# Optimization experiments

Hardware: AMD Instinct MI355X
Metric: run time of the kernel (lower is better)

## Reference

```python
import jax, jax.numpy as jnp
import numpy as np

BS, SLEN, DIM, HID, E, TOPK = 4, 2048, 2048, 1792, 8, 2


def setup_inputs() -> dict:
    key = jax.random.key(0)
    ks = jax.random.split(key, 9)
    s = 0.02  # trunc_normal-style init scale
    return {
        "x": jax.random.normal(ks[0], (BS, SLEN, DIM), jnp.float32),
        "gate_w": jax.random.normal(ks[1], (DIM, E), jnp.float32) * s,
        "w1": jax.random.normal(ks[2], (E, DIM, HID), jnp.float32) * s,
        "w2": jax.random.normal(ks[3], (E, HID, DIM), jnp.float32) * s,
        "w3": jax.random.normal(ks[4], (E, DIM, HID), jnp.float32) * s,
        "sw1": jax.random.normal(ks[5], (DIM, HID), jnp.float32) * s,
        "sw2": jax.random.normal(ks[6], (HID, DIM), jnp.float32) * s,
        "sw3": jax.random.normal(ks[7], (DIM, HID), jnp.float32) * s,
        "expert_bias": jnp.zeros((E,), jnp.float32),
    }


def reference(x, gate_w, w1, w2, w3, sw1, sw2, sw3, expert_bias):
    bs, slen, dim = x.shape
    T = bs * slen
    xf = x.reshape(T, dim)

    # --- TokenChoiceTopKRouter ---
    scores = jax.nn.softmax((xf @ gate_w).astype(jnp.float32), axis=-1)  # [T, E]
    _, sel = jax.lax.top_k(scores + expert_bias[None, :], TOPK)          # [T, K] expert ids
    top_scores = jnp.take_along_axis(scores, sel, axis=1)                # [T, K] (bias-free scores)
    flat_sel = sel.reshape(-1)                                           # [T*K]
    counts = jnp.bincount(flat_sel, length=E).astype(jnp.int32)          # tokens per expert
    order = jnp.argsort(flat_sel, stable=True)                           # group tokens by expert
    top_scores_sorted = top_scores.reshape(-1)[order]                    # [T*K]
    token_idx = order // TOPK                                            # source token per routed row

    # --- dispatch: gather + scale by router weight ---
    routed_in = xf[token_idx] * top_scores_sorted[:, None]               # [T*K, dim]

    # --- GroupedExperts: grouped GEMM SiLU-gated FFN ---
    h = jax.nn.silu(jax.lax.ragged_dot(routed_in, w1, counts)) \
        * jax.lax.ragged_dot(routed_in, w3, counts)                      # [T*K, hid]
    routed_out = jax.lax.ragged_dot(h, w2, counts)                       # [T*K, dim]

    # --- shared expert (single-expert FFN over all tokens) ---
    out = (jax.nn.silu(xf @ sw1) * (xf @ sw3)) @ sw2                     # [T, dim]

    # --- combine: scatter-add routed outputs back to tokens ---
    out = out.at[token_idx].add(routed_out)
    return out.reshape(bs, slen, dim)
```

## Files before the change

kernel.cpp:

```cpp
#include <hip/hip_runtime.h>

typedef unsigned short u16;
typedef unsigned int u32;

#define TOK   8192
#define DIMK  2048
#define HIDN  1792
#define NEXP  8
#define NPAIR 16384
#define MAXROWS 17408
#define MAXTILES 136

typedef float f32x4 __attribute__((ext_vector_type(4)));
typedef __bf16 bf16x8 __attribute__((ext_vector_type(8)));

__device__ __forceinline__ u16 f2bf(float f) {
    u32 u = __float_as_uint(f);
    u += 0x7fffu + ((u >> 16) & 1u);
    return (u16)(u >> 16);
}

__device__ __forceinline__ void gll16(const void* g, void* l) {
    __builtin_amdgcn_global_load_lds((__attribute__((address_space(1))) void*)(g),
                                     (__attribute__((address_space(3))) void*)(l),
                                     16, 0, 0);
}

__global__ void transpose_f2bf(const float* __restrict__ In, u16* __restrict__ Out,
                               int R, int C) {
    __shared__ float tile[64 * 65];
    size_t moff = (size_t)blockIdx.z * R * C;
    const float* in = In + moff;
    u16* out = Out + moff;
    int c0 = blockIdx.x * 64, r0 = blockIdx.y * 64;
    int tid = threadIdx.x;
#pragma unroll
    for (int p = 0; p < 16; ++p) {
        int idx = tid + p * 256;
        int r = idx >> 6, c = idx & 63;
        tile[r * 65 + c] = in[(size_t)(r0 + r) * C + c0 + c];
    }
    __syncthreads();
#pragma unroll
    for (int p = 0; p < 8; ++p) {
        int idx = (tid + p * 256) * 2;
        int ro = idx >> 6;
        int co = idx & 63;
        float v0 = tile[co * 65 + ro];
        float v1 = tile[(co + 1) * 65 + ro];
        u32 u = (u32)f2bf(v0) | ((u32)f2bf(v1) << 16);
        *(u32*)&out[(size_t)(c0 + ro) * R + r0 + co] = u;
    }
}

__global__ void cvt_f2bf(const float* __restrict__ in, u16* __restrict__ out, int n8) {
    int i = blockIdx.x * 256 + threadIdx.x;
    if (i >= n8) return;
    const float4* p = (const float4*)in;
    float4 a = p[2 * i], b = p[2 * i + 1];
    union { u16 us[8]; uint4 u4; } o;
    o.us[0] = f2bf(a.x); o.us[1] = f2bf(a.y); o.us[2] = f2bf(a.z); o.us[3] = f2bf(a.w);
    o.us[4] = f2bf(b.x); o.us[5] = f2bf(b.y); o.us[6] = f2bf(b.z); o.us[7] = f2bf(b.w);
    ((uint4*)out)[i] = o.u4;
}

__global__ void router_k(const float* __restrict__ x, const float* __restrict__ gw,
                         const float* __restrict__ ebias, int* __restrict__ sel,
                         float* __restrict__ scor, int* __restrict__ pos,
                         int* __restrict__ counts) {
    int wave = threadIdx.x >> 6, lane = threadIdx.x & 63;
    int t = blockIdx.x * 4 + wave;
    const float* xr = x + (size_t)t * DIMK;
    float acc[8];
#pragma unroll
    for (int e = 0; e < 8; ++e) acc[e] = 0.f;
    for (int i = lane; i < DIMK; i += 64) {
        float xv = xr[i];
        float4 g0 = *(const float4*)(gw + (size_t)i * 8);
        float4 g1 = *(const float4*)(gw + (size_t)i * 8 + 4);
        acc[0] += xv * g0.x; acc[1] += xv * g0.y; acc[2] += xv * g0.z; acc[3] += xv * g0.w;
        acc[4] += xv * g1.x; acc[5] += xv * g1.y; acc[6] += xv * g1.z; acc[7] += xv * g1.w;
    }
#pragma unroll
    for (int off = 32; off; off >>= 1)
#pragma unroll
        for (int e = 0; e < 8; ++e) acc[e] += __shfl_xor(acc[e], off, 64);
    if (lane == 0) {
        float mx = acc[0];
#pragma unroll
        for (int e = 1; e < 8; ++e) mx = fmaxf(mx, acc[e]);
        float pv[8], psum = 0.f;
#pragma unroll
        for (int e = 0; e < 8; ++e) { pv[e] = __expf(acc[e] - mx); psum += pv[e]; }
        float inv = 1.f / psum;
        float bb[8];
#pragma unroll
        for (int e = 0; e < 8; ++e) { pv[e] *= inv; bb[e] = pv[e] + ebias[e]; }
        int e0 = 0;
#pragma unroll
        for (int e = 1; e < 8; ++e) if (bb[e] > bb[e0]) e0 = e;
        int e1 = (e0 == 0) ? 1 : 0;
#pragma unroll
        for (int e = 0; e < 8; ++e) if (e != e0 && bb[e] > bb[e1]) e1 = e;
        int i0 = t * 2, i1 = t * 2 + 1;
        sel[i0] = e0; sel[i1] = e1;
        scor[i0] = pv[e0]; scor[i1] = pv[e1];
        pos[i0] = atomicAdd(&counts[e0], 1);
        pos[i1] = atomicAdd(&counts[e1], 1);
    }
}

__global__ void scan_k(const int* __restrict__ counts, int* __restrict__ seg,
                       int* __restrict__ tile_e, int* __restrict__ tile_r0,
                       int* __restrict__ ntile) {
    if (threadIdx.x == 0 && blockIdx.x == 0) {
        int off = 0, nt = 0;
        for (int e = 0; e < NEXP; ++e) {
            seg[e] = off;
            int c = counts[e];
            int tiles = (c + 127) >> 7;
            for (int j = 0; j < tiles; ++j) { tile_e[nt] = e; tile_r0[nt] = off + (j << 7); ++nt; }
            off += tiles << 7;
        }
        *ntile = nt;
    }
}

__global__ void dispatch_k(const float* __restrict__ x, const int* __restrict__ sel,
                           const float* __restrict__ scor, const int* __restrict__ pos,
                           const int* __restrict__ counts, const int* __restrict__ seg,
                           u32* __restrict__ rin, int* __restrict__ tok) {
    int b = blockIdx.x;
    if (b < NPAIR) {
        int t = b >> 1;
        int e = sel[b];
        float s = scor[b];
        int row = seg[e] + pos[b];
        const float2* xr = (const float2*)(x + (size_t)t * DIMK);
        u32* orow = rin + (size_t)row * (DIMK / 2);
        for (int i = threadIdx.x; i < DIMK / 2; i += 256) {
            float2 v = xr[i];
            orow[i] = (u32)f2bf(v.x * s) | ((u32)f2bf(v.y * s) << 16);
        }
        if (threadIdx.x == 0) tok[row] = t;
    } else {
        int pb = b - NPAIR;
        int e = pb >> 7, j = pb & 127;
        int c = counts[e];
        int al = (c + 127) & ~127;
        if (c + j < al) {
            int row = seg[e] + c + j;
            u32* orow = rin + (size_t)row * (DIMK / 2);
            for (int i = threadIdx.x; i < DIMK / 2; i += 256) orow[i] = 0u;
            if (threadIdx.x == 0) tok[row] = -1;
        }
    }
}

template <bool GROUPED>
__launch_bounds__(256, 2)
__global__ void gemm_h(const u16* __restrict__ A, const u16* __restrict__ B1g,
                       const u16* __restrict__ B3g, u16* __restrict__ H,
                       const int* __restrict__ tile_e, const int* __restrict__ tile_r0,
                       const int* __restrict__ ntile) {
    constexpr int Kd = DIMK;
    constexpr int Nd = HIDN;
    __shared__ u16 As[128 * 32];
    __shared__ u16 B1s[128 * 32];
    __shared__ u16 B3s[128 * 32];
    int bx = blockIdx.x;
    int r0; size_t woff = 0;
    if constexpr (GROUPED) {
        if (bx >= *ntile) return;
        r0 = tile_r0[bx];
        woff = (size_t)tile_e[bx] * (size_t)Nd * Kd;
    } else {
        r0 = bx * 128;
    }
    int c0 = blockIdx.y * 128;
    int tid = threadIdx.x, wave = tid >> 6, lane = tid & 63;
    int srow = wave * 16 + (lane >> 2);
    int skc = (lane & 3) * 8;
    const u16* gA0 = A + (size_t)(r0 + srow) * Kd + skc;
    const u16* gA1 = gA0 + (size_t)64 * Kd;
    const u16* gB1a = B1g + woff + (size_t)(c0 + srow) * Kd + skc;
    const u16* gB1b = gB1a + (size_t)64 * Kd;
    const u16* gB3a = B3g + woff + (size_t)(c0 + srow) * Kd + skc;
    const u16* gB3b = gB3a + (size_t)64 * Kd;
    char* lA0 = (char*)As + wave * 1024;   char* lA1 = (char*)As + 4096 + wave * 1024;
    char* lB1a = (char*)B1s + wave * 1024; char* lB1b = (char*)B1s + 4096 + wave * 1024;
    char* lB3a = (char*)B3s + wave * 1024; char* lB3b = (char*)B3s + 4096 + wave * 1024;

    int wr = wave >> 1, wc = wave & 1;
    int fr = lane & 15, fq = lane >> 4;
    const u16* fA = As + (wr * 64 + fr) * 32 + fq * 8;
    const u16* fB1 = B1s + (wc * 64 + fr) * 32 + fq * 8;
    const u16* fB3 = B3s + (wc * 64 + fr) * 32 + fq * 8;

    f32x4 acc1[4][4], acc3[4][4];
    f32x4 zz = {0.f, 0.f, 0.f, 0.f};
#pragma unroll
    for (int m = 0; m < 4; ++m)
#pragma unroll
        for (int n = 0; n < 4; ++n) { acc1[m][n] = zz; acc3[m][n] = zz; }

    for (int kt = 0; kt < Kd / 32; ++kt) {
        int ko = kt * 32;
        gll16(gA0 + ko, lA0);  gll16(gA1 + ko, lA1);
        gll16(gB1a + ko, lB1a); gll16(gB1b + ko, lB1b);
        gll16(gB3a + ko, lB3a); gll16(gB3b + ko, lB3b);
        __syncthreads();
        bf16x8 aF[4], b1F[4], b3F[4];
#pragma unroll
        for (int m = 0; m < 4; ++m) aF[m] = *(const bf16x8*)(fA + m * 16 * 32);
#pragma unroll
        for (int n = 0; n < 4; ++n) {
            b1F[n] = *(const bf16x8*)(fB1 + n * 16 * 32);
            b3F[n] = *(const bf16x8*)(fB3 + n * 16 * 32);
        }
#pragma unroll
        for (int m = 0; m < 4; ++m)
#pragma unroll
            for (int n = 0; n < 4; ++n) {
                acc1[m][n] = __builtin_amdgcn_mfma_f32_16x16x32_bf16(aF[m], b1F[n], acc1[m][n], 0, 0, 0);
                acc3[m][n] = __builtin_amdgcn_mfma_f32_16x16x32_bf16(aF[m], b3F[n], acc3[m][n], 0, 0, 0);
            }
        __syncthreads();
    }
#pragma unroll
    for (int m = 0; m < 4; ++m) {
#pragma unroll
        for (int n = 0; n < 4; ++n) {
            int gcol = c0 + wc * 64 + n * 16 + fr;
#pragma unroll
            for (int i = 0; i < 4; ++i) {
                int grow = r0 + wr * 64 + m * 16 + fq * 4 + i;
                float p1 = acc1[m][n][i], p3 = acc3[m][n][i];
                float h = p1 * p3 / (1.f + __expf(-p1));
                H[(size_t)grow * Nd + gcol] = f2bf(h);
            }
        }
    }
}

template <int MODE>
__launch_bounds__(256, 2)
__global__ void gemm_o(const u16* __restrict__ A, const u16* __restrict__ Bg,
                       float* __restrict__ Out,
                       const int* __restrict__ tile_e, const int* __restrict__ tile_r0,
                       const int* __restrict__ ntile, const int* __restrict__ tok) {
    constexpr int Kd = HIDN;
    constexpr int Nd = DIMK;
    __shared__ u16 As[128 * 32];
    __shared__ u16 Bs[128 * 32];
    int bx = blockIdx.x;
    int r0; size_t woff = 0;
    if constexpr (MODE == 1) {
        if (bx >= *ntile) return;
        r0 = tile_r0[bx];
        woff = (size_t)tile_e[bx] * (size_t)Nd * Kd;
    } else {
        r0 = bx * 128;
    }
    int c0 = blockIdx.y * 128;
    int tid = threadIdx.x, wave = tid >> 6, lane = tid & 63;
    int srow = wave * 16 + (lane >> 2);
    int skc = (lane & 3) * 8;
    const u16* gA0 = A + (size_t)(r0 + srow) * Kd + skc;
    const u16* gA1 = gA0 + (size_t)64 * Kd;
    const u16* gB0 = Bg + woff + (size_t)(c0 + srow) * Kd + skc;
    const u16* gB1 = gB0 + (size_t)64 * Kd;
    char* lA0 = (char*)As + wave * 1024; char* lA1 = (char*)As + 4096 + wave * 1024;
    char* lB0 = (char*)Bs + wave * 1024; char* lB1 = (char*)Bs + 4096 + wave * 1024;
    int wr = wave >> 1, wc = wave & 1;
    int fr = lane & 15, fq = lane >> 4;
    const u16* fA = As + (wr * 64 + fr) * 32 + fq * 8;
    const u16* fB = Bs + (wc * 64 + fr) * 32 + fq * 8;
    f32x4 acc[4][4];
    f32x4 zz = {0.f, 0.f, 0.f, 0.f};
#pragma unroll
    for (int m = 0; m < 4; ++m)
#pragma unroll
        for (int n = 0; n < 4; ++n) acc[m][n] = zz;
    for (int kt = 0; kt < Kd / 32; ++kt) {
        int ko = kt * 32;
        gll16(gA0 + ko, lA0); gll16(gA1 + ko, lA1);
        gll16(gB0 + ko, lB0); gll16(gB1 + ko, lB1);
        __syncthreads();
        bf16x8 aF[4], bF[4];
#pragma unroll
        for (int m = 0; m < 4; ++m) aF[m] = *(const bf16x8*)(fA + m * 16 * 32);
#pragma unroll
        for (int n = 0; n < 4; ++n) bF[n] = *(const bf16x8*)(fB + n * 16 * 32);
#pragma unroll
        for (int m = 0; m < 4; ++m)
#pragma unroll
            for (int n = 0; n < 4; ++n)
                acc[m][n] = __builtin_amdgcn_mfma_f32_16x16x32_bf16(aF[m], bF[n], acc[m][n], 0, 0, 0);
        __syncthreads();
    }
#pragma unroll
    for (int m = 0; m < 4; ++m) {
        int tkv[4];
        if constexpr (MODE == 1) {
#pragma unroll
            for (int i = 0; i < 4; ++i) tkv[i] = tok[r0 + wr * 64 + m * 16 + fq * 4 + i];
        }
#pragma unroll
        for (int n = 0; n < 4; ++n) {
            int gcol = c0 + wc * 64 + n * 16 + fr;
#pragma unroll
            for (int i = 0; i < 4; ++i) {
                float v = acc[m][n][i];
                if constexpr (MODE == 0) {
                    int grow = r0 + wr * 64 + m * 16 + fq * 4 + i;
                    Out[(size_t)grow * Nd + gcol] = v;
                } else {
                    int t2 = tkv[i];
                    if (t2 >= 0) atomicAdd(&Out[(size_t)t2 * Nd + gcol], v);
                }
            }
        }
    }
}

extern "C" void kernel_launch(void* const* d_in, const int* in_sizes, int n_in,
                              void* d_out, int out_size, void* d_ws, size_t ws_size,
                              hipStream_t stream) {
    const float* x    = (const float*)d_in[0];
    const float* gw   = (const float*)d_in[1];
    const float* w1   = (const float*)d_in[2];
    const float* w2   = (const float*)d_in[3];
    const float* w3   = (const float*)d_in[4];
    const float* sw1  = (const float*)d_in[5];
    const float* sw2  = (const float*)d_in[6];
    const float* sw3  = (const float*)d_in[7];
    const float* ebias= (const float*)d_in[8];
    float* out = (float*)d_out;

    char* p = (char*)d_ws;
    auto alloc = [&](size_t b) -> char* {
        char* r = p; p += (b + 255) & ~(size_t)255; return r;
    };
    u16* w1b  = (u16*)alloc((size_t)NEXP * HIDN * DIMK * 2);
    u16* w3b  = (u16*)alloc((size_t)NEXP * HIDN * DIMK * 2);
    u16* w2b  = (u16*)alloc((size_t)NEXP * DIMK * HIDN * 2);
    u16* sw1b = (u16*)alloc((size_t)HIDN * DIMK * 2);
    u16* sw3b = (u16*)alloc((size_t)HIDN * DIMK * 2);
    u16* sw2b = (u16*)alloc((size_t)DIMK * HIDN * 2);
    u16* xb   = (u16*)alloc((size_t)TOK * DIMK * 2);
    u16* rin  = (u16*)alloc((size_t)MAXROWS * DIMK * 2);
    u16* hbuf = (u16*)alloc((size_t)MAXROWS * HIDN * 2);
    int* sel    = (int*)alloc(NPAIR * 4);
    float* scor = (float*)alloc(NPAIR * 4);
    int* pos    = (int*)alloc(NPAIR * 4);
    int* counts = (int*)alloc(64);
    int* seg    = (int*)alloc(64);
    int* tile_e = (int*)alloc(256 * 4);
    int* tile_r0= (int*)alloc(256 * 4);
    int* ntile  = (int*)alloc(64);
    int* tok    = (int*)alloc(MAXROWS * 4);

    hipMemsetAsync(counts, 0, NEXP * 4, stream);

    transpose_f2bf<<<dim3(HIDN / 64, DIMK / 64, NEXP), 256, 0, stream>>>(w1, w1b, DIMK, HIDN);
    transpose_f2bf<<<dim3(HIDN / 64, DIMK / 64, NEXP), 256, 0, stream>>>(w3, w3b, DIMK, HIDN);
    transpose_f2bf<<<dim3(DIMK / 64, HIDN / 64, NEXP), 256, 0, stream>>>(w2, w2b, HIDN, DIMK);
    transpose_f2bf<<<dim3(HIDN / 64, DIMK / 64, 1), 256, 0, stream>>>(sw1, sw1b, DIMK, HIDN);
    transpose_f2bf<<<dim3(HIDN / 64, DIMK / 64, 1), 256, 0, stream>>>(sw3, sw3b, DIMK, HIDN);
    transpose_f2bf<<<dim3(DIMK / 64, HIDN / 64, 1), 256, 0, stream>>>(sw2, sw2b, HIDN, DIMK);

    cvt_f2bf<<<(TOK * DIMK / 8 + 255) / 256, 256, 0, stream>>>(x, xb, TOK * DIMK / 8);
    router_k<<<TOK / 4, 256, 0, stream>>>(x, gw, ebias, sel, scor, pos, counts);
    scan_k<<<1, 64, 0, stream>>>(counts, seg, tile_e, tile_r0, ntile);
    dispatch_k<<<NPAIR + NEXP * 128, 256, 0, stream>>>(x, sel, scor, pos, counts, seg,
                                                       (u32*)rin, tok);

    gemm_h<false><<<dim3(TOK / 128, HIDN / 128), 256, 0, stream>>>(
        xb, sw1b, sw3b, hbuf, nullptr, nullptr, nullptr);
    gemm_o<0><<<dim3(TOK / 128, DIMK / 128), 256, 0, stream>>>(
        hbuf, sw2b, out, nullptr, nullptr, nullptr, nullptr);

    gemm_h<true><<<dim3(MAXTILES, HIDN / 128), 256, 0, stream>>>(
        rin, w1b, w3b, hbuf, tile_e, tile_r0, ntile);
    gemm_o<1><<<dim3(MAXTILES, DIMK / 128), 256, 0, stream>>>(
        hbuf, w2b, out, tile_e, tile_r0, ntile, tok);
}
```

Baseline: 1.440 ms.

## Replace GEMMs with 256x256 pipelined kernel, interleaved w1/w3 and merged shared expert

Replaces the four 128x128 GEMM kernels with one templated 256x256-tile, 512-thread GEMM. It double-buffers LDS with direct global-to-LDS loads and XOR swizzling, and splits each k-step into phases separated by barriers and setprio. w1 and w3 are interleaved in 16-row groups into one concatenated weight, so a single B stream yields both gate and up products. The shared expert is treated as a ninth expert, so it shares the grouped launch for the first layer. The intent is better data reuse and MFMA utilization. The cost is larger padding (256-row tiles), more LDS per block and heavier register pressure.

```diff
diff --git a/kernel.cpp b/kernel.cpp
--- a/kernel.cpp
+++ b/kernel.cpp
@@ -3,13 +3,15 @@
 typedef unsigned short u16;
 typedef unsigned int u32;
 
-#define TOK   8192
-#define DIMK  2048
-#define HIDN  1792
-#define NEXP  8
-#define NPAIR 16384
-#define MAXROWS 17408
-#define MAXTILES 136
+#define TOK    8192
+#define DIMK   2048
+#define HIDN   1792
+#define NCAT   3584
+#define NEXP   8
+#define NPAIR  16384
+#define RROWS  18432
+#define CROWS  26624
+#define MAXMT  104
 
 typedef float f32x4 __attribute__((ext_vector_type(4)));
 typedef __bf16 bf16x8 __attribute__((ext_vector_type(8)));
@@ -19,7 +21,6 @@
     u += 0x7fffu + ((u >> 16) & 1u);
     return (u16)(u >> 16);
 }
-
 __device__ __forceinline__ void gll16(const void* g, void* l) {
     __builtin_amdgcn_global_load_lds((__attribute__((address_space(1))) void*)(g),
                                      (__attribute__((address_space(3))) void*)(l),
@@ -27,11 +28,11 @@
 }
 
 __global__ void transpose_f2bf(const float* __restrict__ In, u16* __restrict__ Out,
-                               int R, int C) {
+                               int R, int C, size_t in_z, size_t out_z, size_t out_off,
+                               int ilv) {
     __shared__ float tile[64 * 65];
-    size_t moff = (size_t)blockIdx.z * R * C;
-    const float* in = In + moff;
-    u16* out = Out + moff;
+    const float* in = In + (size_t)blockIdx.z * in_z;
+    u16* out = Out + (size_t)blockIdx.z * out_z + out_off;
     int c0 = blockIdx.x * 64, r0 = blockIdx.y * 64;
     int tid = threadIdx.x;
 #pragma unroll
@@ -49,7 +50,9 @@
         float v0 = tile[co * 65 + ro];
         float v1 = tile[(co + 1) * 65 + ro];
         u32 u = (u32)f2bf(v0) | ((u32)f2bf(v1) << 16);
-        *(u32*)&out[(size_t)(c0 + ro) * R + r0 + co] = u;
+        int orow = c0 + ro;
+        if (ilv) orow = ((orow & ~15) << 1) + (ilv == 2 ? 16 : 0) + (orow & 15);
+        *(u32*)&out[(size_t)orow * R + r0 + co] = u;
     }
 }
 
@@ -111,18 +114,21 @@
 }
 
 __global__ void scan_k(const int* __restrict__ counts, int* __restrict__ seg,
-                       int* __restrict__ tile_e, int* __restrict__ tile_r0,
-                       int* __restrict__ ntile) {
+                       int* __restrict__ mt_e, int* __restrict__ mt_r0,
+                       int* __restrict__ nmt, int* __restrict__ nrows) {
     if (threadIdx.x == 0 && blockIdx.x == 0) {
-        int off = 0, nt = 0;
+        int ntl = 0;
+        for (int i = 0; i < TOK / 256; ++i) { mt_e[ntl] = 8; mt_r0[ntl] = i * 256; ++ntl; }
+        int off = TOK;
         for (int e = 0; e < NEXP; ++e) {
             seg[e] = off;
             int c = counts[e];
-            int tiles = (c + 127) >> 7;
-            for (int j = 0; j < tiles; ++j) { tile_e[nt] = e; tile_r0[nt] = off + (j << 7); ++nt; }
-            off += tiles << 7;
-        }
-        *ntile = nt;
+            int tl = (c + 255) >> 8;
+            for (int j = 0; j < tl; ++j) { mt_e[ntl] = e; mt_r0[ntl] = off + (j << 8); ++ntl; }
+            off += tl << 8;
+        }
+        *nmt = ntl;
+        *nrows = off;
     }
 }
 
@@ -137,7 +143,7 @@
         float s = scor[b];
         int row = seg[e] + pos[b];
         const float2* xr = (const float2*)(x + (size_t)t * DIMK);
-        u32* orow = rin + (size_t)row * (DIMK / 2);
+        u32* orow = rin + (size_t)(row - TOK) * (DIMK / 2);
         for (int i = threadIdx.x; i < DIMK / 2; i += 256) {
             float2 v = xr[i];
             orow[i] = (u32)f2bf(v.x * s) | ((u32)f2bf(v.y * s) << 16);
@@ -145,180 +151,175 @@
         if (threadIdx.x == 0) tok[row] = t;
     } else {
         int pb = b - NPAIR;
-        int e = pb >> 7, j = pb & 127;
+        int e = pb >> 8, j = pb & 255;
         int c = counts[e];
-        int al = (c + 127) & ~127;
+        int al = (c + 255) & ~255;
         if (c + j < al) {
             int row = seg[e] + c + j;
-            u32* orow = rin + (size_t)row * (DIMK / 2);
+            u32* orow = rin + (size_t)(row - TOK) * (DIMK / 2);
             for (int i = threadIdx.x; i < DIMK / 2; i += 256) orow[i] = 0u;
             if (threadIdx.x == 0) tok[row] = -1;
         }
     }
 }
 
-template <bool GROUPED>
-__launch_bounds__(256, 2)
-__global__ void gemm_h(const u16* __restrict__ A, const u16* __restrict__ B1g,
-                       const u16* __restrict__ B3g, u16* __restrict__ H,
-                       const int* __restrict__ tile_e, const int* __restrict__ tile_r0,
-                       const int* __restrict__ ntile) {
-    constexpr int Kd = DIMK;
-    constexpr int Nd = HIDN;
-    __shared__ u16 As[128 * 32];
-    __shared__ u16 B1s[128 * 32];
-    __shared__ u16 B3s[128 * 32];
-    int bx = blockIdx.x;
-    int r0; size_t woff = 0;
-    if constexpr (GROUPED) {
-        if (bx >= *ntile) return;
-        r0 = tile_r0[bx];
-        woff = (size_t)tile_e[bx] * (size_t)Nd * Kd;
+#define LDA(mh, b) { \
+    _Pragma("unroll") for (int m_ = 0; m_ < 4; ++m_) \
+    _Pragma("unroll") for (int ks_ = 0; ks_ < 2; ++ks_) \
+        aF[mh][m_][ks_] = *(const bf16x8*)(&lds[b][0][0] + aRd + ((mh)*4 + m_) * 2048 + ks_ * 64); }
+#define LDB(nh, b) { \
+    _Pragma("unroll") for (int n_ = 0; n_ < 2; ++n_) \
+    _Pragma("unroll") for (int ks_ = 0; ks_ < 2; ++ks_) \
+        bF[n_][ks_] = *(const bf16x8*)(&lds[b][1][0] + bRd + ((nh)*2 + n_) * 2048 + ks_ * 64); }
+#define MFMAQ(mh, nh) { \
+    _Pragma("unroll") for (int m_ = 0; m_ < 4; ++m_) \
+    _Pragma("unroll") for (int n_ = 0; n_ < 2; ++n_) \
+    _Pragma("unroll") for (int ks_ = 0; ks_ < 2; ++ks_) \
+        acc[(mh)*4 + m_][(nh)*2 + n_] = __builtin_amdgcn_mfma_f32_16x16x32_bf16( \
+            aF[mh][m_][ks_], bF[n_][ks_], acc[(mh)*4 + m_][(nh)*2 + n_], 0, 0, 0); }
+#define SA(kt, half, b) do { \
+    const char* s_ = gA + (size_t)(half) * (128 * ABS) + (size_t)(kt) * 128; \
+    char* d_ = &lds[b][0][0] + (half) * 16384 + t16; \
+    gll16(s_, d_); gll16(s_ + 64 * ABS, d_ + 8192); } while (0)
+#define SB(kt, half, b) do { \
+    const char* s_ = gB + (size_t)(half) * (128 * BBS) + (size_t)(kt) * 128; \
+    char* d_ = &lds[b][1][0] + (half) * 16384 + t16; \
+    gll16(s_, d_); gll16(s_ + 64 * BBS, d_ + 8192); } while (0)
+#define PH_SYNC() \
+    __builtin_amdgcn_s_barrier(); \
+    asm volatile("s_waitcnt lgkmcnt(0)" ::: "memory"); \
+    __builtin_amdgcn_sched_barrier(0); \
+    __builtin_amdgcn_s_setprio(1)
+#define PH_END() \
+    __builtin_amdgcn_s_setprio(0); \
+    __builtin_amdgcn_s_barrier()
+
+template <int KD, int ND, int ASTR, int EPI>
+__launch_bounds__(512, 2)
+__global__ void gemm256(const u16* __restrict__ A0, const u16* __restrict__ A1,
+                        const u16* __restrict__ Bcat, void* __restrict__ Obase,
+                        const int* __restrict__ mt_e, const int* __restrict__ mt_r0,
+                        const int* __restrict__ nmt, const int* __restrict__ tok,
+                        int tile_off) {
+    int my = blockIdx.y + tile_off;
+    if (my >= *nmt) return;
+    const int e = mt_e[my];
+    const int r0 = mt_r0[my];
+    const int c0 = blockIdx.x * 256;
+
+    const u16* Ab;
+    if constexpr (EPI == 0)
+        Ab = (r0 < TOK) ? (A0 + (size_t)r0 * ASTR) : (A1 + (size_t)(r0 - TOK) * ASTR);
+    else
+        Ab = A0 + (size_t)r0 * ASTR;
+    const u16* Bb = Bcat + (size_t)e * ND * KD + (size_t)c0 * KD;
+
+    __shared__ char lds[2][2][32768];
+
+    const int t = threadIdx.x;
+    const int lane = t & 63;
+    const int wid = t >> 6;
+    const int wr = wid >> 2, wc = wid & 3;
+    const int fr = lane & 15, fq = lane >> 4;
+    const int sbit = ((fr >> 2) & 1) << 5;
+    const int aRd = ((wr * 128 + fr) * 128 + fq * 16) ^ sbit;
+    const int bRd = ((wc * 64 + fr) * 128 + fq * 16) ^ sbit;
+    const int t16 = t * 16;
+    constexpr size_t ABS = (size_t)ASTR * 2;
+    constexpr size_t BBS = (size_t)KD * 2;
+    const int scb = ((t & 7) * 16) ^ (((t >> 5) & 1) << 5);
+    const char* gA = (const char*)Ab + (size_t)(t >> 3) * ABS + scb;
+    const char* gB = (const char*)Bb + (size_t)(t >> 3) * BBS + scb;
+
+    f32x4 acc[8][4];
+    const f32x4 zz = {0.f, 0.f, 0.f, 0.f};
+#pragma unroll
+    for (int m = 0; m < 8; ++m)
+#pragma unroll
+        for (int n = 0; n < 4; ++n) acc[m][n] = zz;
+    bf16x8 aF[2][4][2], bF[2][2];
+
+    constexpr int NT = KD / 64;
+    constexpr int NITER = NT / 2;
+
+    SA(0, 0, 0); SA(0, 1, 0); SB(0, 0, 0); SB(0, 1, 0);
+    SA(1, 0, 1); SA(1, 1, 1);
+    asm volatile("s_waitcnt vmcnt(4)" ::: "memory");
+    __builtin_amdgcn_s_barrier();
+
+#pragma unroll 1
+    for (int it = 0; it < NITER; ++it) {
+        const int t0 = 2 * it;
+        const bool pf = (t0 + 2 < NT);
+        LDA(0, 0); LDB(0, 0);
+        SB(t0 + 1, 0, 1);
+        PH_SYNC(); MFMAQ(0, 0); PH_END();
+        LDA(1, 0);
+        SB(t0 + 1, 1, 1);
+        PH_SYNC(); MFMAQ(1, 0); PH_END();
+        LDB(1, 0);
+        if (pf) SA(t0 + 2, 0, 0);
+        PH_SYNC(); MFMAQ(0, 1); PH_END();
+        if (pf) { SA(t0 + 2, 1, 0); asm volatile("s_waitcnt vmcnt(4)" ::: "memory"); }
+        else    { asm volatile("s_waitcnt vmcnt(0)" ::: "memory"); }
+        PH_SYNC(); MFMAQ(1, 1); PH_END();
+        LDA(0, 1); LDB(0, 1);
+        if (pf) SB(t0 + 2, 0, 0);
+        PH_SYNC(); MFMAQ(0, 0); PH_END();
+        LDA(1, 1);
+        if (pf) SB(t0 + 2, 1, 0);
+        PH_SYNC(); MFMAQ(1, 0); PH_END();
+        LDB(1, 1);
+        if (pf) SA(t0 + 3, 0, 1);
+        PH_SYNC(); MFMAQ(0, 1); PH_END();
+        if (pf) { SA(t0 + 3, 1, 1); asm volatile("s_waitcnt vmcnt(4)" ::: "memory"); }
+        PH_SYNC(); MFMAQ(1, 1); PH_END();
+    }
+
+    if constexpr (EPI == 0) {
+        u16* H = (u16*)Obase;
+        constexpr int HST = ND / 2;
+#pragma unroll
+        for (int m = 0; m < 8; ++m) {
+#pragma unroll
+            for (int n = 0; n < 4; n += 2) {
+                int gc = (c0 + wc * 64 + n * 16) / 2 + fr;
+#pragma unroll
+                for (int i = 0; i < 4; ++i) {
+                    int gr = r0 + wr * 128 + m * 16 + fq * 4 + i;
+                    float p1 = acc[m][n][i], p3 = acc[m][n + 1][i];
+                    float h = p1 * p3 / (1.f + __expf(-p1));
+                    H[(size_t)gr * HST + gc] = f2bf(h);
+                }
+            }
+        }
+    } else if constexpr (EPI == 1) {
+        float* O = (float*)Obase;
+#pragma unroll
+        for (int m = 0; m < 8; ++m)
+#pragma unroll
+            for (int n = 0; n < 4; ++n) {
+                int gc = c0 + wc * 64 + n * 16 + fr;
+#pragma unroll
+                for (int i = 0; i < 4; ++i) {
+                    int gr = r0 + wr * 128 + m * 16 + fq * 4 + i;
+                    O[(size_t)gr * ND + gc] = acc[m][n][i];
+                }
+            }
     } else {
-        r0 = bx * 128;
-    }
-    int c0 = blockIdx.y * 128;
-    int tid = threadIdx.x, wave = tid >> 6, lane = tid & 63;
-    int srow = wave * 16 + (lane >> 2);
-    int skc = (lane & 3) * 8;
-    const u16* gA0 = A + (size_t)(r0 + srow) * Kd + skc;
-    const u16* gA1 = gA0 + (size_t)64 * Kd;
-    const u16* gB1a = B1g + woff + (size_t)(c0 + srow) * Kd + skc;
-    const u16* gB1b = gB1a + (size_t)64 * Kd;
-    const u16* gB3a = B3g + woff + (size_t)(c0 + srow) * Kd + skc;
-    const u16* gB3b = gB3a + (size_t)64 * Kd;
-    char* lA0 = (char*)As + wave * 1024;   char* lA1 = (char*)As + 4096 + wave * 1024;
-    char* lB1a = (char*)B1s + wave * 1024; char* lB1b = (char*)B1s + 4096 + wave * 1024;
-    char* lB3a = (char*)B3s + wave * 1024; char* lB3b = (char*)B3s + 4096 + wave * 1024;
-
-    int wr = wave >> 1, wc = wave & 1;
-    int fr = lane & 15, fq = lane >> 4;
-    const u16* fA = As + (wr * 64 + fr) * 32 + fq * 8;
-    const u16* fB1 = B1s + (wc * 64 + fr) * 32 + fq * 8;
-    const u16* fB3 = B3s + (wc * 64 + fr) * 32 + fq * 8;
-
-    f32x4 acc1[4][4], acc3[4][4];
-    f32x4 zz = {0.f, 0.f, 0.f, 0.f};
-#pragma unroll
-    for (int m = 0; m < 4; ++m)
-#pragma unroll
-        for (int n = 0; n < 4; ++n) { acc1[m][n] = zz; acc3[m][n] = zz; }
-
-    for (int kt = 0; kt < Kd / 32; ++kt) {
-        int ko = kt * 32;
-        gll16(gA0 + ko, lA0);  gll16(gA1 + ko, lA1);
-        gll16(gB1a + ko, lB1a); gll16(gB1b + ko, lB1b);
-        gll16(gB3a + ko, lB3a); gll16(gB3b + ko, lB3b);
-        __syncthreads();
-        bf16x8 aF[4], b1F[4], b3F[4];
-#pragma unroll
-        for (int m = 0; m < 4; ++m) aF[m] = *(const bf16x8*)(fA + m * 16 * 32);
-#pragma unroll
-        for (int n = 0; n < 4; ++n) {
-            b1F[n] = *(const bf16x8*)(fB1 + n * 16 * 32);
-            b3F[n] = *(const bf16x8*)(fB3 + n * 16 * 32);
-        }
-#pragma unroll
-        for (int m = 0; m < 4; ++m)
+        float* O = (float*)Obase;
+#pragma unroll
+        for (int m = 0; m < 8; ++m) {
+            int tk[4];
+#pragma unroll
+            for (int i = 0; i < 4; ++i)
+                tk[i] = tok[r0 + wr * 128 + m * 16 + fq * 4 + i];
 #pragma unroll
             for (int n = 0; n < 4; ++n) {
-                acc1[m][n] = __builtin_amdgcn_mfma_f32_16x16x32_bf16(aF[m], b1F[n], acc1[m][n], 0, 0, 0);
-                acc3[m][n] = __builtin_amdgcn_mfma_f32_16x16x32_bf16(aF[m], b3F[n], acc3[m][n], 0, 0, 0);
-            }
-        __syncthreads();
-    }
-#pragma unroll
-    for (int m = 0; m < 4; ++m) {
-#pragma unroll
-        for (int n = 0; n < 4; ++n) {
-            int gcol = c0 + wc * 64 + n * 16 + fr;
-#pragma unroll
-            for (int i = 0; i < 4; ++i) {
-                int grow = r0 + wr * 64 + m * 16 + fq * 4 + i;
-                float p1 = acc1[m][n][i], p3 = acc3[m][n][i];
-                float h = p1 * p3 / (1.f + __expf(-p1));
-                H[(size_t)grow * Nd + gcol] = f2bf(h);
-            }
-        }
-    }
-}
-
-template <int MODE>
-__launch_bounds__(256, 2)
-__global__ void gemm_o(const u16* __restrict__ A, const u16* __restrict__ Bg,
-                       float* __restrict__ Out,
-                       const int* __restrict__ tile_e, const int* __restrict__ tile_r0,
-                       const int* __restrict__ ntile, const int* __restrict__ tok) {
-    constexpr int Kd = HIDN;
-    constexpr int Nd = DIMK;
-    __shared__ u16 As[128 * 32];
-    __shared__ u16 Bs[128 * 32];
-    int bx = blockIdx.x;
-    int r0; size_t woff = 0;
-    if constexpr (MODE == 1) {
-        if (bx >= *ntile) return;
-        r0 = tile_r0[bx];
-        woff = (size_t)tile_e[bx] * (size_t)Nd * Kd;
-    } else {
-        r0 = bx * 128;
-    }
-    int c0 = blockIdx.y * 128;
-    int tid = threadIdx.x, wave = tid >> 6, lane = tid & 63;
-    int srow = wave * 16 + (lane >> 2);
-    int skc = (lane & 3) * 8;
-    const u16* gA0 = A + (size_t)(r0 + srow) * Kd + skc;
-    const u16* gA1 = gA0 + (size_t)64 * Kd;
-    const u16* gB0 = Bg + woff + (size_t)(c0 + srow) * Kd + skc;
-    const u16* gB1 = gB0 + (size_t)64 * Kd;
-    char* lA0 = (char*)As + wave * 1024; char* lA1 = (char*)As + 4096 + wave * 1024;
-    char* lB0 = (char*)Bs + wave * 1024; char* lB1 = (char*)Bs + 4096 + wave * 1024;
-    int wr = wave >> 1, wc = wave & 1;
-    int fr = lane & 15, fq = lane >> 4;
-    const u16* fA = As + (wr * 64 + fr) * 32 + fq * 8;
-    const u16* fB = Bs + (wc * 64 + fr) * 32 + fq * 8;
-    f32x4 acc[4][4];
-    f32x4 zz = {0.f, 0.f, 0.f, 0.f};
-#pragma unroll
-    for (int m = 0; m < 4; ++m)
-#pragma unroll
-        for (int n = 0; n < 4; ++n) acc[m][n] = zz;
-    for (int kt = 0; kt < Kd / 32; ++kt) {
-        int ko = kt * 32;
-        gll16(gA0 + ko, lA0); gll16(gA1 + ko, lA1);
-        gll16(gB0 + ko, lB0); gll16(gB1 + ko, lB1);
-        __syncthreads();
-        bf16x8 aF[4], bF[4];
-#pragma unroll
-        for (int m = 0; m < 4; ++m) aF[m] = *(const bf16x8*)(fA + m * 16 * 32);
-#pragma unroll
-        for (int n = 0; n < 4; ++n) bF[n] = *(const bf16x8*)(fB + n * 16 * 32);
-#pragma unroll
-        for (int m = 0; m < 4; ++m)
-#pragma unroll
-            for (int n = 0; n < 4; ++n)
-                acc[m][n] = __builtin_amdgcn_mfma_f32_16x16x32_bf16(aF[m], bF[n], acc[m][n], 0, 0, 0);
-        __syncthreads();
-    }
-#pragma unroll
-    for (int m = 0; m < 4; ++m) {
-        int tkv[4];
-        if constexpr (MODE == 1) {
-#pragma unroll
-            for (int i = 0; i < 4; ++i) tkv[i] = tok[r0 + wr * 64 + m * 16 + fq * 4 + i];
-        }
-#pragma unroll
-        for (int n = 0; n < 4; ++n) {
-            int gcol = c0 + wc * 64 + n * 16 + fr;
-#pragma unroll
-            for (int i = 0; i < 4; ++i) {
-                float v = acc[m][n][i];
-                if constexpr (MODE == 0) {
-                    int grow = r0 + wr * 64 + m * 16 + fq * 4 + i;
-                    Out[(size_t)grow * Nd + gcol] = v;
-                } else {
-                    int t2 = tkv[i];
-                    if (t2 >= 0) atomicAdd(&Out[(size_t)t2 * Nd + gcol], v);
-                }
+                int gc = c0 + wc * 64 + n * 16 + fr;
+#pragma unroll
+                for (int i = 0; i < 4; ++i)
+                    if (tk[i] >= 0) atomicAdd(&O[(size_t)tk[i] * ND + gc], acc[m][n][i]);
             }
         }
     }
@@ -342,47 +343,49 @@
     auto alloc = [&](size_t b) -> char* {
         char* r = p; p += (b + 255) & ~(size_t)255; return r;
     };
-    u16* w1b  = (u16*)alloc((size_t)NEXP * HIDN * DIMK * 2);
-    u16* w3b  = (u16*)alloc((size_t)NEXP * HIDN * DIMK * 2);
-    u16* w2b  = (u16*)alloc((size_t)NEXP * DIMK * HIDN * 2);
-    u16* sw1b = (u16*)alloc((size_t)HIDN * DIMK * 2);
-    u16* sw3b = (u16*)alloc((size_t)HIDN * DIMK * 2);
-    u16* sw2b = (u16*)alloc((size_t)DIMK * HIDN * 2);
-    u16* xb   = (u16*)alloc((size_t)TOK * DIMK * 2);
-    u16* rin  = (u16*)alloc((size_t)MAXROWS * DIMK * 2);
-    u16* hbuf = (u16*)alloc((size_t)MAXROWS * HIDN * 2);
+    u16* wcat  = (u16*)alloc((size_t)9 * NCAT * DIMK * 2);
+    u16* w2cat = (u16*)alloc((size_t)9 * DIMK * HIDN * 2);
+    u16* xb    = (u16*)alloc((size_t)TOK * DIMK * 2);
+    u16* rin   = (u16*)alloc((size_t)RROWS * DIMK * 2);
+    u16* hbuf  = (u16*)alloc((size_t)CROWS * HIDN * 2);
     int* sel    = (int*)alloc(NPAIR * 4);
     float* scor = (float*)alloc(NPAIR * 4);
     int* pos    = (int*)alloc(NPAIR * 4);
     int* counts = (int*)alloc(64);
     int* seg    = (int*)alloc(64);
-    int* tile_e = (int*)alloc(256 * 4);
-    int* tile_r0= (int*)alloc(256 * 4);
-    int* ntile  = (int*)alloc(64);
-    int* tok    = (int*)alloc(MAXROWS * 4);
+    int* mt_e   = (int*)alloc(MAXMT * 4);
+    int* mt_r0  = (int*)alloc(MAXMT * 4);
+    int* nmt    = (int*)alloc(64);
+    int* nrows  = (int*)alloc(64);
+    int* tok    = (int*)alloc(CROWS * 4);
 
     hipMemsetAsync(counts, 0, NEXP * 4, stream);
 
-    transpose_f2bf<<<dim3(HIDN / 64, DIMK / 64, NEXP), 256, 0, stream>>>(w1, w1b, DIMK, HIDN);
-    transpose_f2bf<<<dim3(HIDN / 64, DIMK / 64, NEXP), 256, 0, stream>>>(w3, w3b, DIMK, HIDN);
-    transpose_f2bf<<<dim3(DIMK / 64, HIDN / 64, NEXP), 256, 0, stream>>>(w2, w2b, HIDN, DIMK);
-    transpose_f2bf<<<dim3(HIDN / 64, DIMK / 64, 1), 256, 0, stream>>>(sw1, sw1b, DIMK, HIDN);
-    transpose_f2bf<<<dim3(HIDN / 64, DIMK / 64, 1), 256, 0, stream>>>(sw3, sw3b, DIMK, HIDN);
-    transpose_f2bf<<<dim3(DIMK / 64, HIDN / 64, 1), 256, 0, stream>>>(sw2, sw2b, HIDN, DIMK);
+    size_t wz = (size_t)NCAT * DIMK;
+    size_t w2z = (size_t)DIMK * HIDN;
+    transpose_f2bf<<<dim3(HIDN/64, DIMK/64, NEXP), 256, 0, stream>>>(
+        w1, wcat, DIMK, HIDN, (size_t)DIMK*HIDN, wz, 0, 1);
+    transpose_f2bf<<<dim3(HIDN/64, DIMK/64, NEXP), 256, 0, stream>>>(
+        w3, wcat, DIMK, HIDN, (size_t)DIMK*HIDN, wz, 0, 2);
+    transpose_f2bf<<<dim3(HIDN/64, DIMK/64, 1), 256, 0, stream>>>(
+        sw1, wcat, DIMK, HIDN, 0, 0, 8*wz, 1);
+    transpose_f2bf<<<dim3(HIDN/64, DIMK/64, 1), 256, 0, stream>>>(
+        sw3, wcat, DIMK, HIDN, 0, 0, 8*wz, 2);
+    transpose_f2bf<<<dim3(DIMK/64, HIDN/64, NEXP), 256, 0, stream>>>(
+        w2, w2cat, HIDN, DIMK, (size_t)HIDN*DIMK, w2z, 0, 0);
+    transpose_f2bf<<<dim3(DIMK/64, HIDN/64, 1), 256, 0, stream>>>(
+        sw2, w2cat, HIDN, DIMK, 0, 0, 8*w2z, 0);
 
     cvt_f2bf<<<(TOK * DIMK / 8 + 255) / 256, 256, 0, stream>>>(x, xb, TOK * DIMK / 8);
     router_k<<<TOK / 4, 256, 0, stream>>>(x, gw, ebias, sel, scor, pos, counts);
-    scan_k<<<1, 64, 0, stream>>>(counts, seg, tile_e, tile_r0, ntile);
-    dispatch_k<<<NPAIR + NEXP * 128, 256, 0, stream>>>(x, sel, scor, pos, counts, seg,
+    scan_k<<<1, 64, 0, stream>>>(counts, seg, mt_e, mt_r0, nmt, nrows);
+    dispatch_k<<<NPAIR + NEXP * 256, 256, 0, stream>>>(x, sel, scor, pos, counts, seg,
                                                        (u32*)rin, tok);
 
-    gemm_h<false><<<dim3(TOK / 128, HIDN / 128), 256, 0, stream>>>(
-        xb, sw1b, sw3b, hbuf, nullptr, nullptr, nullptr);
-    gemm_o<0><<<dim3(TOK / 128, DIMK / 128), 256, 0, stream>>>(
-        hbuf, sw2b, out, nullptr, nullptr, nullptr, nullptr);
-
-    gemm_h<true><<<dim3(MAXTILES, HIDN / 128), 256, 0, stream>>>(
-        rin, w1b, w3b, hbuf, tile_e, tile_r0, ntile);
-    gemm_o<1><<<dim3(MAXTILES, DIMK / 128), 256, 0, stream>>>(
-        hbuf, w2b, out, tile_e, tile_r0, ntile, tok);
-}
+    gemm256<DIMK, NCAT, DIMK, 0><<<dim3(NCAT/256, MAXMT), 512, 0, stream>>>(
+        xb, rin, wcat, hbuf, mt_e, mt_r0, nmt, nullptr, 0);
+    gemm256<HIDN, DIMK, HIDN, 1><<<dim3(DIMK/256, TOK/256), 512, 0, stream>>>(
+        hbuf, nullptr, w2cat, out, mt_e, mt_r0, nmt, nullptr, 0);
+    gemm256<HIDN, DIMK, HIDN, 2><<<dim3(DIMK/256, MAXMT - TOK/256), 512, 0, stream>>>(
+        hbuf, nullptr, w2cat, out, mt_e, mt_r0, nmt, tok, TOK/256);
+}
```

Result: faster. 1.343 ms (-6.7%).
